# Kernel tuning notes

Hardware: AMD Instinct MI355X
Metric: run time of the kernel (lower is better)

## Reference

```python
import jax, jax.numpy as jnp
import numpy as np

B, DIM, CH = 4, 128, 256      # dim=channels[0], channel=channels[1]
H = W = 256                   # high-res spatial
H0 = W0 = 128                 # low-res spatial (H/2)
NH = 8                        # num_heads
HD = DIM // NH                # head_dim = 16
RD = HD // 2                  # DANE reduction=2 -> 8


def _ln(x, g, b, eps=1e-5):
    m = x.mean(-1, keepdims=True)
    v = ((x - m) ** 2).mean(-1, keepdims=True)
    return (x - m) * jax.lax.rsqrt(v + eps) * g + b


def setup_inputs() -> dict:
    key = jax.random.key(0)
    ks = jax.random.split(key, 14)
    f = lambda k, s: jax.random.normal(k, s, jnp.float32) * 0.02
    return dict(
        x_l=jax.random.normal(ks[0], (B, CH, H0, W0), jnp.float32),
        x_r=jax.random.normal(ks[1], (B, CH, H0, W0), jnp.float32),
        x_l_high=jax.random.normal(ks[2], (B, DIM, H, W), jnp.float32),
        x_r_high=jax.random.normal(ks[3], (B, DIM, H, W), jnp.float32),
        Wq=f(ks[4], (DIM, DIM)), bq=jnp.zeros((DIM,), jnp.float32),
        Wqv=f(ks[5], (DIM, DIM)), bqv=jnp.zeros((DIM,), jnp.float32),
        Wk=f(ks[6], (DIM, CH)), bk=jnp.zeros((DIM,), jnp.float32),
        Wv=f(ks[7], (DIM, CH)), bv=jnp.zeros((DIM,), jnp.float32),
        Wp=f(ks[8], (DIM, DIM)), bp=jnp.zeros((DIM,), jnp.float32),
        ln_g=jnp.ones((DIM,), jnp.float32), ln_b=jnp.zeros((DIM,), jnp.float32),
        d_ln1_g=jnp.ones((HD,), jnp.float32), d_ln1_b=jnp.zeros((HD,), jnp.float32),
        d_ws=f(ks[9], (1, HD)),
        d_w1=f(ks[10], (RD, HD)),
        d_ln2_g=jnp.ones((RD,), jnp.float32), d_ln2_b=jnp.zeros((RD,), jnp.float32),
        d_w2=f(ks[11], (HD, RD)),
    )


def _cross_attn(source, target, Wq, bq, Wqv, bqv, Wk, bk, Wv, bv, Wp, bp,
                ln_g, ln_b, d_ln1_g, d_ln1_b, d_ws, d_w1, d_ln2_g, d_ln2_b, d_w2):
    b_, c, hh, ww = source.shape
    _, c0, h0, w0 = target.shape
    n0 = h0 * w0
    h, d = NH, c // NH
    # 2x2 patchify high-res: (B,C,H0,2,W0,2) -> (B,N0,4,C)
    src = source.reshape(b_, c, h0, 2, w0, 2).transpose(0, 2, 4, 3, 5, 1).reshape(b_, n0, 4, c)
    # low-res target as single token per patch: (B,N0,1,C0)
    tgt = target.reshape(b_, c0, n0).transpose(0, 2, 1)[:, :, None, :]
    q = (src @ Wq.T + bq).reshape(b_, n0, 4, h, d).swapaxes(2, 3)   # (B,N0,h,4,d)
    vq = (src @ Wqv.T + bqv).reshape(b_, n0, 4, h, d).swapaxes(2, 3)
    k = (tgt @ Wk.T + bk).reshape(b_, n0, 1, h, d).swapaxes(2, 3)   # (B,N0,h,1,d)
    v = (tgt @ Wv.T + bv).reshape(b_, n0, 1, h, d).swapaxes(2, 3)
    attn = jnp.einsum('bnhqd,bnhkd->bnhqk', q, k) * (d ** -0.5)     # (B,N0,h,4,1)
    attn = jax.nn.softmax(attn, axis=-2)                            # softmax over the 4-patch axis
    # DANE spatial gate: LN + Linear(d->1) on q, averaged over the 4-patch axis
    sm = (_ln(q, d_ln1_g, d_ln1_b) @ d_ws.T).mean(axis=(3, 4))      # (B,N0,h)
    # DANE channel gate: mean of k over N0, then bottleneck MLP
    km = k.mean(axis=1)                                             # (B,h,1,d)
    cm = jax.nn.silu(km @ d_w1.T)
    cm = _ln(cm, d_ln2_g, d_ln2_b) @ d_w2.T                         # (B,h,1,d)
    w_gate = jax.nn.sigmoid(sm[:, :, :, None, None] + cm[:, None])  # (B,N0,h,1,d)
    x = (1.0 - w_gate) * (attn * v) * 4.0 + w_gate * vq             # (B,N0,h,4,d)
    x = x.swapaxes(2, 3).reshape(b_, n0, 4, c)
    x = _ln(x @ Wp.T + bp, ln_g, ln_b)
    # un-patchify back to (B,C,H,W)
    x = x.reshape(b_, h0, w0, 2, 2, c).transpose(0, 5, 1, 3, 2, 4).reshape(b_, c, hh, ww)
    return x


def reference(x_l, x_r, x_l_high, x_r_high, Wq, bq, Wqv, bqv, Wk, bk, Wv, bv, Wp, bp,
              ln_g, ln_b, d_ln1_g, d_ln1_b, d_ws, d_w1, d_ln2_g, d_ln2_b, d_w2):
    w = (Wq, bq, Wqv, bqv, Wk, bk, Wv, bv, Wp, bp, ln_g, ln_b,
         d_ln1_g, d_ln1_b, d_ws, d_w1, d_ln2_g, d_ln2_b, d_w2)
    # PAFM.fuse (eval mode: DropPath=identity, UsePatch=False => patch=Identity)
    out_l = x_l_high + _cross_attn(x_l_high, x_l, *w)
    out_r = x_r_high + _cross_attn(x_r_high, x_r, *w)
    return (out_l, out_r)
```

## Files before the change

### kernel.cpp

```cpp
#include <hip/hip_runtime.h>
#include <hip/hip_bf16.h>
#include <math.h>


typedef short short8 __attribute__((ext_vector_type(8)));
typedef float f32x4 __attribute__((ext_vector_type(4)));

__device__ __forceinline__ unsigned bf16r(float x) {
    unsigned u = __float_as_uint(x);
    return (u + 0x7FFFu + ((u >> 16) & 1u)) >> 16;
}
__device__ __forceinline__ unsigned pack2(float a, float b) {
    return bf16r(a) | (bf16r(b) << 16);
}
__device__ __forceinline__ float ubf(unsigned short h) {
    return __uint_as_float(((unsigned)h) << 16);
}

__global__ __launch_bounds__(256) void mean_kernel(const float* __restrict__ x_l,
                                                   const float* __restrict__ x_r,
                                                   float* __restrict__ ws_mean) {
    int bid = blockIdx.x;
    const float* src = (bid >= 1024) ? x_r : x_l;
    const float* p = src + (size_t)(bid & 1023) * 16384;
    int t = threadIdx.x;
    float acc = 0.f;
    #pragma unroll 4
    for (int i = t; i < 16384; i += 256) acc += p[i];
    #pragma unroll
    for (int off = 32; off > 0; off >>= 1) acc += __shfl_down(acc, off, 64);
    __shared__ float red[4];
    if ((t & 63) == 0) red[t >> 6] = acc;
    __syncthreads();
    if (t == 0) ws_mean[bid] = (red[0] + red[1] + red[2] + red[3]) * (1.f / 16384.f);
}

__global__ __launch_bounds__(128) void cm_kernel(const float* __restrict__ ws_mean,
                                                 float* __restrict__ ws_cm,
                                                 const float* __restrict__ Wk,
                                                 const float* __restrict__ bk,
                                                 const float* __restrict__ d_w1,
                                                 const float* __restrict__ d_ln2_g,
                                                 const float* __restrict__ d_ln2_b,
                                                 const float* __restrict__ d_w2) {
    int sb = blockIdx.x;
    __shared__ float km[128];
    int o = threadIdx.x;
    const float* mu = ws_mean + sb * 256;
    float acc = bk[o];
    for (int c = 0; c < 256; ++c) acc = fmaf(Wk[o * 256 + c], mu[c], acc);
    km[o] = acc;
    __syncthreads();
    int h = o >> 4, d = o & 15;
    float t1[8];
    #pragma unroll
    for (int r = 0; r < 8; ++r) {
        float a = 0.f;
        #pragma unroll
        for (int dd = 0; dd < 16; ++dd) a = fmaf(d_w1[r * 16 + dd], km[h * 16 + dd], a);
        t1[r] = a / (1.f + expf(-a));
    }
    float m = 0.f;
    #pragma unroll
    for (int r = 0; r < 8; ++r) m += t1[r];
    m *= 0.125f;
    float v = 0.f;
    #pragma unroll
    for (int r = 0; r < 8; ++r) { float df = t1[r] - m; v = fmaf(df, df, v); }
    float rstd = rsqrtf(v * 0.125f + 1e-5f);
    float cmv = 0.f;
    #pragma unroll
    for (int r = 0; r < 8; ++r)
        cmv = fmaf((t1[r] - m) * rstd * d_ln2_g[r] + d_ln2_b[r], d_w2[d * 8 + r], cmv);
    ws_cm[sb * 128 + o] = cmv;
}

__global__ __launch_bounds__(256) void wprep(const float* __restrict__ Wq,
                                             const float* __restrict__ Wqv,
                                             const float* __restrict__ Wk,
                                             const float* __restrict__ Wv,
                                             const float* __restrict__ Wp,
                                             unsigned short* __restrict__ wsp) {
    int bid = blockIdx.x, t = threadIdx.x;
    if (bid < 64) {
        const float* src = (bid < 32) ? Wk : Wv;
        unsigned short* dst = wsp + ((bid < 32) ? 0 : 32768);
        int base = (bid & 31) * 1024;
        #pragma unroll
        for (int i = 0; i < 4; ++i) {
            int el = base + t + 256 * i;
            int q = el >> 13, rem = el & 8191, op = rem >> 8, col = rem & 255;
            dst[q * 8192 + op * 256 + (col ^ ((op & 7) << 3))] =
                (unsigned short)bf16r(src[(q * 32 + op) * 256 + col]);
        }
    } else {
        int g = (bid - 64) >> 4;
        const float* src = (g == 0) ? Wq : (g == 1) ? Wqv : Wp;
        unsigned short* dst = wsp + 65536 + g * 16384;
        int base = ((bid - 64) & 15) * 1024;
        #pragma unroll
        for (int i = 0; i < 4; ++i) {
            int el = base + t + 256 * i;
            int hf = el >> 13, rem = el & 8191, op = rem >> 7, col = rem & 127;
            dst[hf * 8192 + op * 128 + (col ^ ((op & 7) << 3))] =
                (unsigned short)bf16r(src[(hf * 64 + op) * 128 + col]);
        }
    }
}

#define O_XH0 0
#define O_XH1 16384
#define O_XC  32768
#define O_WB  49152
#define O_K   57344
#define O_V   65536
#define O_LG  73728
#define O_SM  75776
#define LDS_U16 76800

__device__ __forceinline__ short8 frag(const unsigned short* lds, int off, int row, int k, int C2) {
    return *(const short8*)&lds[off + row * C2 + (k ^ ((row & 7) << 3))];
}

template<int R, int C2>
__device__ __forceinline__ void stageA(const float* __restrict__ g, size_t cstride,
                                       unsigned short* lds, int off, int t) {
    #pragma unroll
    for (int it = 0; it < (R * (C2 / 2)) / 512; ++it) {
        int idx = t + it * 512;
        int rr = idx & (R - 1);
        int cp = idx / R;
        float a0 = g[(size_t)(2 * cp) * cstride + rr];
        float a1 = g[(size_t)(2 * cp + 1) * cstride + rr];
        int col = (2 * cp) ^ ((rr & 7) << 3);
        *(unsigned*)&lds[off + rr * C2 + col] = pack2(a0, a1);
    }
}

__device__ __forceinline__ void stageW16(const unsigned short* __restrict__ src,
                                         unsigned short* lds, int t) {
    #pragma unroll
    for (int c = 0; c < 2; ++c) {
        int u = (c * 512 + t) * 8;
        *(short8*)&lds[O_WB + u] = *(const short8*)&src[u];
    }
}

#define ZERO4(A) do { _Pragma("unroll") for (int z_ = 0; z_ < 4; ++z_) A[z_] = (f32x4){0.f,0.f,0.f,0.f}; } while (0)

#define KVQ(WOFF, BIAS, OBASE, ODST) do {                                          \
    stageW16(wsp + (WOFF), lds, t);                                                \
    __syncthreads();                                                               \
    f32x4 a_ = (f32x4){0.f,0.f,0.f,0.f};                                           \
    int nt_ = w >> 2, mt_ = w & 3;                                                 \
    _Pragma("unroll")                                                              \
    for (int kc_ = 0; kc_ < 8; ++kc_) {                                            \
      short8 af_ = frag(lds, O_XH0, 16 * mt_ + lm, kc_ * 32 + lg * 8, 256);        \
      short8 bf_ = frag(lds, O_WB, 16 * nt_ + lm, kc_ * 32 + lg * 8, 256);         \
      a_ = __builtin_amdgcn_mfma_f32_16x16x32_bf16(af_, bf_, a_, 0, 0, 0);         \
    }                                                                              \
    { int o_ = (OBASE) + 16 * nt_ + lm; float bb_ = (BIAS)[o_];                    \
      _Pragma("unroll")                                                            \
      for (int r_ = 0; r_ < 4; ++r_) {                                             \
        int tok_ = 16 * mt_ + 4 * lg + r_;                                         \
        lds[(ODST) + tok_ * 128 + (o_ ^ ((tok_ & 7) << 3))] = (unsigned short)bf16r(a_[r_] + bb_); \
      } }                                                                          \
    __syncthreads();                                                               \
  } while (0)

#define GEMM128(ACC, XOFF) do {                                                    \
    _Pragma("unroll")                                                              \
    for (int kc_ = 0; kc_ < 4; ++kc_) {                                            \
      short8 af_ = frag(lds, (XOFF), 16 * w + lm, kc_ * 32 + lg * 8, 128);         \
      _Pragma("unroll")                                                            \
      for (int n_ = 0; n_ < 4; ++n_) {                                             \
        short8 bf_ = frag(lds, O_WB, 16 * n_ + lm, kc_ * 32 + lg * 8, 128);        \
        ACC[n_] = __builtin_amdgcn_mfma_f32_16x16x32_bf16(af_, bf_, ACC[n_], 0, 0, 0); \
      } }                                                                          \
  } while (0)

#define CONSUME(ACC, DY, NH) do {                                                  \
    _Pragma("unroll")                                                              \
    for (int n_ = 0; n_ < 4; ++n_) {                                               \
      int nt_ = 4 * (NH) + n_;                                                     \
      int o_ = 16 * nt_ + lm;                                                      \
      float bias_ = bq[o_];                                                        \
      float sd01_ = 0.f, sd23_ = 0.f;                                              \
      _Pragma("unroll")                                                            \
      for (int r_ = 0; r_ < 4; ++r_) {                                             \
        int row_ = 16 * w + 4 * lg + r_;                                           \
        int tok_ = row_ >> 1;                                                      \
        float q_ = ACC[n_][r_] + bias_;                                            \
        float kv_ = ubf(lds[O_K + tok_ * 128 + (o_ ^ ((tok_ & 7) << 3))]);         \
        float t0_ = q_, t1_ = q_ * q_, t2_ = q_ * gw, t3_ = q_ * kv_;              \
        _Pragma("unroll")                                                          \
        for (int d_ = 1; d_ < 16; d_ <<= 1) {                                      \
          t0_ += __shfl_xor(t0_, d_, 64); t1_ += __shfl_xor(t1_, d_, 64);          \
          t2_ += __shfl_xor(t2_, d_, 64); t3_ += __shfl_xor(t3_, d_, 64);          \
        }                                                                          \
        float mn_ = t0_ * 0.0625f;                                                 \
        float rs_ = rsqrtf(t1_ * 0.0625f - mn_ * mn_ + 1e-5f);                     \
        float sdt_ = rs_ * (t2_ - mn_ * S1) + S2;                                  \
        if (r_ < 2) sd01_ += sdt_; else sd23_ += sdt_;                             \
        if (lm == r_) lds[O_LG + ((DY) * 128 + row_) * 8 + nt_] = (unsigned short)bf16r(t3_ * 0.25f); \
      }                                                                            \
      if (lm == 0) smf[(8 * w + 2 * lg) * 8 + nt_]     += sd01_;                   \
      if (lm == 1) smf[(8 * w + 2 * lg + 1) * 8 + nt_] += sd23_;                   \
    } } while (0)

#define COMBINE(ACC, DY, NH) do {                                                  \
    _Pragma("unroll")                                                              \
    for (int n_ = 0; n_ < 4; ++n_) {                                               \
      int nt_ = 4 * (NH) + n_;                                                     \
      int o_ = 16 * nt_ + lm;                                                      \
      float bias_ = bqv[o_];                                                       \
      float cmv_ = cmp[o_];                                                        \
      _Pragma("unroll")                                                            \
      for (int r_ = 0; r_ < 4; ++r_) {                                             \
        int row_ = 16 * w + 4 * lg + r_;                                           \
        int jj_ = row_ >> 1;                                                       \
        float vq_ = ACC[n_][r_] + bias_;                                           \
        float aw_ = ubf(lds[O_LG + ((DY) * 128 + row_) * 8 + nt_]);                \
        float vv_ = ubf(lds[O_V + jj_ * 128 + (o_ ^ ((jj_ & 7) << 3))]);           \
        float wg_ = 1.f / (1.f + __expf(-(smf[jj_ * 8 + nt_] + cmv_)));            \
        float xc_ = (1.f - wg_) * aw_ * vv_ * 4.f + wg_ * vq_;                     \
        lds[O_XC + row_ * 128 + (o_ ^ ((row_ & 7) << 3))] = (unsigned short)bf16r(xc_); \
      } } } while (0)

__global__ __launch_bounds__(512, 2) void pafm_v5(
    const float* __restrict__ x_l,  const float* __restrict__ x_r,
    const float* __restrict__ x_lh, const float* __restrict__ x_rh,
    const float* __restrict__ bq,   const float* __restrict__ bqv,
    const float* __restrict__ bk,   const float* __restrict__ bv,
    const float* __restrict__ bp,
    const float* __restrict__ ln_g, const float* __restrict__ ln_b,
    const float* __restrict__ d_ln1_g, const float* __restrict__ d_ln1_b,
    const float* __restrict__ d_wsv,
    const float* __restrict__ ws_cm,
    const unsigned short* __restrict__ wsp,
    float* __restrict__ out) {

    __shared__ unsigned short lds[LDS_U16];
    float* smf = (float*)&lds[O_SM];

    int bid = blockIdx.x;
    int s  = bid >> 10;
    int b  = (bid >> 8) & 3;
    int i0 = (bid >> 1) & 127;
    int j0 = (bid & 1) * 64;

    int t = threadIdx.x, w = t >> 6, l = t & 63, lm = l & 15, lg = l >> 4;

    const float* xlow  = s ? x_r  : x_l;
    const float* xhigh = s ? x_rh : x_lh;
    const float* cmp   = ws_cm + (s * 4 + b) * 128;

    float gw = d_ln1_g[lm] * d_wsv[lm];
    float S1 = gw, S2 = d_ln1_b[lm] * d_wsv[lm];
    #pragma unroll
    for (int d = 1; d < 16; d <<= 1) { S1 += __shfl_xor(S1, d, 64); S2 += __shfl_xor(S2, d, 64); }

    const float* lowb = xlow + ((size_t)(b * 256) * 128 + i0) * 128 + j0;

    smf[t & 511] = 0.f;

    stageA<64, 256>(lowb, 16384, lds, O_XH0, t);
    __syncthreads();
    KVQ(0,     bk, 0,  O_K); KVQ(8192,  bk, 32, O_K);
    KVQ(16384, bk, 64, O_K); KVQ(24576, bk, 96, O_K);
    KVQ(32768, bv, 0,  O_V); KVQ(40960, bv, 32, O_V);
    KVQ(49152, bv, 64, O_V); KVQ(57344, bv, 96, O_V);

    {
        const float* hb0 = xhigh + ((size_t)(b * 128) * 256 + (2 * i0)) * 256 + 2 * j0;
        const float* hb1 = hb0 + 256;
        stageA<128, 128>(hb0, 65536, lds, O_XH0, t);
        stageA<128, 128>(hb1, 65536, lds, O_XH1, t);
    }
    __syncthreads();

    {
        stageW16(wsp + 65536, lds, t);
        __syncthreads();
        { f32x4 q4[4]; ZERO4(q4); GEMM128(q4, O_XH0); CONSUME(q4, 0, 0); }
        { f32x4 q4[4]; ZERO4(q4); GEMM128(q4, O_XH1); CONSUME(q4, 1, 0); }
        __syncthreads();
        stageW16(wsp + 65536 + 8192, lds, t);
        __syncthreads();
        { f32x4 q4[4]; ZERO4(q4); GEMM128(q4, O_XH0); CONSUME(q4, 0, 1); }
        { f32x4 q4[4]; ZERO4(q4); GEMM128(q4, O_XH1); CONSUME(q4, 1, 1); }
        __syncthreads();
    }

    {
        int jj = t >> 3, h = t & 7;
        int r00 = (2 * jj) * 8 + h,       r01 = (2 * jj + 1) * 8 + h;
        int r10 = (128 + 2 * jj) * 8 + h, r11 = (128 + 2 * jj + 1) * 8 + h;
        float l00 = ubf(lds[O_LG + r00]), l01 = ubf(lds[O_LG + r01]);
        float l10 = ubf(lds[O_LG + r10]), l11 = ubf(lds[O_LG + r11]);
        float mx = fmaxf(fmaxf(l00, l01), fmaxf(l10, l11));
        float e00 = __expf(l00 - mx), e01 = __expf(l01 - mx);
        float e10 = __expf(l10 - mx), e11 = __expf(l11 - mx);
        float inv = 1.f / (e00 + e01 + e10 + e11);
        lds[O_LG + r00] = (unsigned short)bf16r(e00 * inv);
        lds[O_LG + r01] = (unsigned short)bf16r(e01 * inv);
        lds[O_LG + r10] = (unsigned short)bf16r(e10 * inv);
        lds[O_LG + r11] = (unsigned short)bf16r(e11 * inv);
        smf[jj * 8 + h] *= 0.25f;
    }
    __syncthreads();

    for (int dy = 0; dy < 2; ++dy) {
        int xoff = dy ? O_XH1 : O_XH0;
        stageW16(wsp + 81920, lds, t);
        __syncthreads();
        { f32x4 v4_[4]; ZERO4(v4_); GEMM128(v4_, xoff); COMBINE(v4_, dy, 0); }
        __syncthreads();
        stageW16(wsp + 81920 + 8192, lds, t);
        __syncthreads();
        { f32x4 v4_[4]; ZERO4(v4_); GEMM128(v4_, xoff); COMBINE(v4_, dy, 1); }
        __syncthreads();

        f32x4 pA[4], pB[4];
        stageW16(wsp + 98304, lds, t);
        __syncthreads();
        ZERO4(pA); GEMM128(pA, O_XC);
        __syncthreads();
        stageW16(wsp + 98304 + 8192, lds, t);
        __syncthreads();
        ZERO4(pB); GEMM128(pB, O_XC);
        __syncthreads();

        float mean_[4], rstd_[4];
        #pragma unroll
        for (int r = 0; r < 4; ++r) {
            float ps = 0.f, pq = 0.f;
            #pragma unroll
            for (int n = 0; n < 4; ++n) {
                float y0 = pA[n][r] + bp[16 * n + lm];
                float y1 = pB[n][r] + bp[64 + 16 * n + lm];
                ps += y0 + y1;
                pq = fmaf(y0, y0, pq); pq = fmaf(y1, y1, pq);
            }
            #pragma unroll
            for (int d = 1; d < 16; d <<= 1) { ps += __shfl_xor(ps, d, 64); pq += __shfl_xor(pq, d, 64); }
            float mn = ps * (1.f / 128.f);
            mean_[r] = mn;
            rstd_[r] = rsqrtf(pq * (1.f / 128.f) - mn * mn + 1e-5f);
        }
        #pragma unroll
        for (int n = 0; n < 4; ++n) {
            int oA = 16 * n + lm, oB = 64 + 16 * n + lm;
            float gA = ln_g[oA], bA = ln_b[oA], biA = bp[oA];
            float gB = ln_g[oB], bB = ln_b[oB], biB = bp[oB];
            #pragma unroll
            for (int r = 0; r < 4; ++r) {
                int row = 16 * w + 4 * lg + r;
                float ynA = (pA[n][r] + biA - mean_[r]) * rstd_[r] * gA + bA;
                float ynB = (pB[n][r] + biB - mean_[r]) * rstd_[r] * gB + bB;
                lds[O_XC + row * 128 + (oA ^ ((row & 31) << 2))] = (unsigned short)bf16r(ynA);
                lds[O_XC + row * 128 + (oB ^ ((row & 31) << 2))] = (unsigned short)bf16r(ynB);
            }
        }
        __syncthreads();
        {
            float* ob = out + (size_t)s * 33554432
                      + ((size_t)(b * 128)) * 65536 + (size_t)(2 * i0 + dy) * 256 + 2 * j0;
            int ph = t & 127, oq = t >> 7;
            #pragma unroll 8
            for (int it = 0; it < 32; ++it) {
                int oo = 4 * it + oq;
                float yn = ubf(lds[O_XC + ph * 128 + (oo ^ ((ph & 31) << 2))]);
                float xh = ubf(lds[xoff + ph * 128 + (oo ^ ((ph & 7) << 3))]);
                ob[(size_t)oo * 65536 + ph] = xh + yn;
            }
        }
        __syncthreads();
    }
}

extern "C" void kernel_launch(void* const* d_in, const int* in_sizes, int n_in,
                              void* d_out, int out_size, void* d_ws, size_t ws_size,
                              hipStream_t stream) {
    const float* x_l   = (const float*)d_in[0];
    const float* x_r   = (const float*)d_in[1];
    const float* x_lh  = (const float*)d_in[2];
    const float* x_rh  = (const float*)d_in[3];
    const float* Wq    = (const float*)d_in[4];
    const float* bq    = (const float*)d_in[5];
    const float* Wqv   = (const float*)d_in[6];
    const float* bqv   = (const float*)d_in[7];
    const float* Wk    = (const float*)d_in[8];
    const float* bk    = (const float*)d_in[9];
    const float* Wv    = (const float*)d_in[10];
    const float* bv    = (const float*)d_in[11];
    const float* Wp    = (const float*)d_in[12];
    const float* bp    = (const float*)d_in[13];
    const float* ln_g  = (const float*)d_in[14];
    const float* ln_b  = (const float*)d_in[15];
    const float* dln1g = (const float*)d_in[16];
    const float* dln1b = (const float*)d_in[17];
    const float* d_wsv = (const float*)d_in[18];
    const float* d_w1  = (const float*)d_in[19];
    const float* dln2g = (const float*)d_in[20];
    const float* dln2b = (const float*)d_in[21];
    const float* d_w2  = (const float*)d_in[22];

    float* out = (float*)d_out;
    float* ws_mean = (float*)d_ws;
    float* ws_cm   = ws_mean + 2048;
    unsigned short* wsp = (unsigned short*)((char*)d_ws + 16384);

    mean_kernel<<<2048, 256, 0, stream>>>(x_l, x_r, ws_mean);
    wprep<<<112, 256, 0, stream>>>(Wq, Wqv, Wk, Wv, Wp, wsp);
    cm_kernel<<<8, 128, 0, stream>>>(ws_mean, ws_cm, Wk, bk, d_w1, dln2g, dln2b, d_w2);
    pafm_v5<<<2048, 512, 0, stream>>>(x_l, x_r, x_lh, x_rh,
                                      bq, bqv, bk, bv, bp, ln_g, ln_b,
                                      dln1g, dln1b, d_wsv, ws_cm, wsp, out);
}
```

Measured before the change: 610.7 us.

## Read weights from global memory and shrink LDS to raise occupancy

```diff
diff --git a/kernel.cpp b/kernel.cpp
--- a/kernel.cpp
+++ b/kernel.cpp
@@ -5,6 +5,7 @@
 
 typedef short short8 __attribute__((ext_vector_type(8)));
 typedef float f32x4 __attribute__((ext_vector_type(4)));
+typedef unsigned uint4v __attribute__((ext_vector_type(4)));
 
 __device__ __forceinline__ unsigned bf16r(float x) {
     unsigned u = __float_as_uint(x);
@@ -108,76 +109,42 @@
     }
 }
 
-#define O_XH0 0
-#define O_XH1 16384
-#define O_XC  32768
-#define O_WB  49152
-#define O_K   57344
-#define O_V   65536
-#define O_LG  73728
-#define O_SM  75776
-#define LDS_U16 76800
+#define O_XA 0
+#define O_K  16384
+#define O_V  24576
+#define O_LG 32768
+#define O_SM 34816
+#define LDS_U16 35840
 
 __device__ __forceinline__ short8 frag(const unsigned short* lds, int off, int row, int k, int C2) {
     return *(const short8*)&lds[off + row * C2 + (k ^ ((row & 7) << 3))];
 }
+__device__ __forceinline__ short8 wfrag(const unsigned short* __restrict__ p, int row, int k, int C2) {
+    return *(const short8*)&p[row * C2 + (k ^ ((row & 7) << 3))];
+}
 
 template<int R, int C2>
-__device__ __forceinline__ void stageA(const float* __restrict__ g, size_t cstride,
-                                       unsigned short* lds, int off, int t) {
-    #pragma unroll
-    for (int it = 0; it < (R * (C2 / 2)) / 512; ++it) {
+__device__ __forceinline__ void stageA16(const float* __restrict__ g, size_t cstride,
+                                         unsigned short* lds, int off, int t) {
+    #pragma unroll
+    for (int it = 0; it < (R * (C2 / 8)) / 512; ++it) {
         int idx = t + it * 512;
         int rr = idx & (R - 1);
-        int cp = idx / R;
-        float a0 = g[(size_t)(2 * cp) * cstride + rr];
-        float a1 = g[(size_t)(2 * cp + 1) * cstride + rr];
-        int col = (2 * cp) ^ ((rr & 7) << 3);
-        *(unsigned*)&lds[off + rr * C2 + col] = pack2(a0, a1);
-    }
-}
-
-__device__ __forceinline__ void stageW16(const unsigned short* __restrict__ src,
-                                         unsigned short* lds, int t) {
-    #pragma unroll
-    for (int c = 0; c < 2; ++c) {
-        int u = (c * 512 + t) * 8;
-        *(short8*)&lds[O_WB + u] = *(const short8*)&src[u];
+        int bc = idx / R;
+        float v0 = g[(size_t)(8 * bc + 0) * cstride + rr];
+        float v1 = g[(size_t)(8 * bc + 1) * cstride + rr];
+        float v2 = g[(size_t)(8 * bc + 2) * cstride + rr];
+        float v3 = g[(size_t)(8 * bc + 3) * cstride + rr];
+        float v4 = g[(size_t)(8 * bc + 4) * cstride + rr];
+        float v5 = g[(size_t)(8 * bc + 5) * cstride + rr];
+        float v6 = g[(size_t)(8 * bc + 6) * cstride + rr];
+        float v7 = g[(size_t)(8 * bc + 7) * cstride + rr];
+        uint4v u = {pack2(v0, v1), pack2(v2, v3), pack2(v4, v5), pack2(v6, v7)};
+        *(uint4v*)&lds[off + rr * C2 + ((bc ^ (rr & 7)) << 3)] = u;
     }
 }
 
 #define ZERO4(A) do { _Pragma("unroll") for (int z_ = 0; z_ < 4; ++z_) A[z_] = (f32x4){0.f,0.f,0.f,0.f}; } while (0)
-
-#define KVQ(WOFF, BIAS, OBASE, ODST) do {                                          \
-    stageW16(wsp + (WOFF), lds, t);                                                \
-    __syncthreads();                                                               \
-    f32x4 a_ = (f32x4){0.f,0.f,0.f,0.f};                                           \
-    int nt_ = w >> 2, mt_ = w & 3;                                                 \
-    _Pragma("unroll")                                                              \
-    for (int kc_ = 0; kc_ < 8; ++kc_) {                                            \
-      short8 af_ = frag(lds, O_XH0, 16 * mt_ + lm, kc_ * 32 + lg * 8, 256);        \
-      short8 bf_ = frag(lds, O_WB, 16 * nt_ + lm, kc_ * 32 + lg * 8, 256);         \
-      a_ = __builtin_amdgcn_mfma_f32_16x16x32_bf16(af_, bf_, a_, 0, 0, 0);         \
-    }                                                                              \
-    { int o_ = (OBASE) + 16 * nt_ + lm; float bb_ = (BIAS)[o_];                    \
-      _Pragma("unroll")                                                            \
-      for (int r_ = 0; r_ < 4; ++r_) {                                             \
-        int tok_ = 16 * mt_ + 4 * lg + r_;                                         \
-        lds[(ODST) + tok_ * 128 + (o_ ^ ((tok_ & 7) << 3))] = (unsigned short)bf16r(a_[r_] + bb_); \
-      } }                                                                          \
-    __syncthreads();                                                               \
-  } while (0)
-
-#define GEMM128(ACC, XOFF) do {                                                    \
-    _Pragma("unroll")                                                              \
-    for (int kc_ = 0; kc_ < 4; ++kc_) {                                            \
-      short8 af_ = frag(lds, (XOFF), 16 * w + lm, kc_ * 32 + lg * 8, 128);         \
-      _Pragma("unroll")                                                            \
-      for (int n_ = 0; n_ < 4; ++n_) {                                             \
-        short8 bf_ = frag(lds, O_WB, 16 * n_ + lm, kc_ * 32 + lg * 8, 128);        \
-        ACC[n_] = __builtin_amdgcn_mfma_f32_16x16x32_bf16(af_, bf_, ACC[n_], 0, 0, 0); \
-      } }                                                                          \
-  } while (0)
 
 #define CONSUME(ACC, DY, NH) do {                                                  \
     _Pragma("unroll")                                                              \
@@ -224,10 +191,10 @@
         float vv_ = ubf(lds[O_V + jj_ * 128 + (o_ ^ ((jj_ & 7) << 3))]);           \
         float wg_ = 1.f / (1.f + __expf(-(smf[jj_ * 8 + nt_] + cmv_)));            \
         float xc_ = (1.f - wg_) * aw_ * vv_ * 4.f + wg_ * vq_;                     \
-        lds[O_XC + row_ * 128 + (o_ ^ ((row_ & 7) << 3))] = (unsigned short)bf16r(xc_); \
+        lds[O_XA + row_ * 128 + (o_ ^ ((row_ & 7) << 3))] = (unsigned short)bf16r(xc_); \
       } } } while (0)
 
-__global__ __launch_bounds__(512, 2) void pafm_v5(
+__global__ __launch_bounds__(512, 4) void pafm_v6(
     const float* __restrict__ x_l,  const float* __restrict__ x_r,
     const float* __restrict__ x_lh, const float* __restrict__ x_rh,
     const float* __restrict__ bq,   const float* __restrict__ bqv,
@@ -261,36 +228,59 @@
     for (int d = 1; d < 16; d <<= 1) { S1 += __shfl_xor(S1, d, 64); S2 += __shfl_xor(S2, d, 64); }
 
     const float* lowb = xlow + ((size_t)(b * 256) * 128 + i0) * 128 + j0;
+    const float* hbase = xhigh + ((size_t)(b * 128) * 256 + 2 * i0) * 256 + 2 * j0;
 
     smf[t & 511] = 0.f;
 
-    stageA<64, 256>(lowb, 16384, lds, O_XH0, t);
+    stageA16<64, 256>(lowb, 16384, lds, O_XA, t);
     __syncthreads();
-    KVQ(0,     bk, 0,  O_K); KVQ(8192,  bk, 32, O_K);
-    KVQ(16384, bk, 64, O_K); KVQ(24576, bk, 96, O_K);
-    KVQ(32768, bv, 0,  O_V); KVQ(40960, bv, 32, O_V);
-    KVQ(49152, bv, 64, O_V); KVQ(57344, bv, 96, O_V);
-
     {
-        const float* hb0 = xhigh + ((size_t)(b * 128) * 256 + (2 * i0)) * 256 + 2 * j0;
-        const float* hb1 = hb0 + 256;
-        stageA<128, 128>(hb0, 65536, lds, O_XH0, t);
-        stageA<128, 128>(hb1, 65536, lds, O_XH1, t);
+        int nt = w >> 2, mt = w & 3;
+        #pragma unroll
+        for (int q = 0; q < 4; ++q) {
+            f32x4 aK = (f32x4){0.f,0.f,0.f,0.f}, aV = (f32x4){0.f,0.f,0.f,0.f};
+            #pragma unroll
+            for (int kc = 0; kc < 8; ++kc) {
+                short8 af = frag(lds, O_XA, 16 * mt + lm, kc * 32 + lg * 8, 256);
+                aK = __builtin_amdgcn_mfma_f32_16x16x32_bf16(
+                        af, wfrag(wsp + q * 8192, 16 * nt + lm, kc * 32 + lg * 8, 256), aK, 0, 0, 0);
+                aV = __builtin_amdgcn_mfma_f32_16x16x32_bf16(
+                        af, wfrag(wsp + 32768 + q * 8192, 16 * nt + lm, kc * 32 + lg * 8, 256), aV, 0, 0, 0);
+            }
+            int o = q * 32 + 16 * nt + lm;
+            float bbk = bk[o], bbv = bv[o];
+            #pragma unroll
+            for (int r = 0; r < 4; ++r) {
+                int tok = 16 * mt + 4 * lg + r;
+                lds[O_K + tok * 128 + (o ^ ((tok & 7) << 3))] = (unsigned short)bf16r(aK[r] + bbk);
+                lds[O_V + tok * 128 + (o ^ ((tok & 7) << 3))] = (unsigned short)bf16r(aV[r] + bbv);
+            }
+        }
+    }
+
+    #pragma unroll 1
+    for (int dy = 0; dy < 2; ++dy) {
+        __syncthreads();
+        stageA16<128, 128>(hbase + dy * 256, 65536, lds, O_XA, t);
+        __syncthreads();
+        f32x4 qA[4], qB[4];
+        ZERO4(qA); ZERO4(qB);
+        #pragma unroll
+        for (int kc = 0; kc < 4; ++kc) {
+            short8 af = frag(lds, O_XA, 16 * w + lm, kc * 32 + lg * 8, 128);
+            #pragma unroll
+            for (int n = 0; n < 4; ++n)
+                qA[n] = __builtin_amdgcn_mfma_f32_16x16x32_bf16(
+                          af, wfrag(wsp + 65536, 16 * n + lm, kc * 32 + lg * 8, 128), qA[n], 0, 0, 0);
+            #pragma unroll
+            for (int n = 0; n < 4; ++n)
+                qB[n] = __builtin_amdgcn_mfma_f32_16x16x32_bf16(
+                          af, wfrag(wsp + 65536 + 8192, 16 * n + lm, kc * 32 + lg * 8, 128), qB[n], 0, 0, 0);
+        }
+        CONSUME(qA, dy, 0);
+        CONSUME(qB, dy, 1);
     }
     __syncthreads();
-
-    {
-        stageW16(wsp + 65536, lds, t);
-        __syncthreads();
-        { f32x4 q4[4]; ZERO4(q4); GEMM128(q4, O_XH0); CONSUME(q4, 0, 0); }
-        { f32x4 q4[4]; ZERO4(q4); GEMM128(q4, O_XH1); CONSUME(q4, 1, 0); }
-        __syncthreads();
-        stageW16(wsp + 65536 + 8192, lds, t);
-        __syncthreads();
-        { f32x4 q4[4]; ZERO4(q4); GEMM128(q4, O_XH0); CONSUME(q4, 0, 1); }
-        { f32x4 q4[4]; ZERO4(q4); GEMM128(q4, O_XH1); CONSUME(q4, 1, 1); }
-        __syncthreads();
-    }
 
     {
         int jj = t >> 3, h = t & 7;
@@ -310,25 +300,43 @@
     }
     __syncthreads();
 
+    #pragma unroll 1
     for (int dy = 0; dy < 2; ++dy) {
-        int xoff = dy ? O_XH1 : O_XH0;
-        stageW16(wsp + 81920, lds, t);
-        __syncthreads();
-        { f32x4 v4_[4]; ZERO4(v4_); GEMM128(v4_, xoff); COMBINE(v4_, dy, 0); }
-        __syncthreads();
-        stageW16(wsp + 81920 + 8192, lds, t);
-        __syncthreads();
-        { f32x4 v4_[4]; ZERO4(v4_); GEMM128(v4_, xoff); COMBINE(v4_, dy, 1); }
+        stageA16<128, 128>(hbase + dy * 256, 65536, lds, O_XA, t);
+        __syncthreads();
+        f32x4 vqA[4], vqB[4];
+        ZERO4(vqA); ZERO4(vqB);
+        #pragma unroll
+        for (int kc = 0; kc < 4; ++kc) {
+            short8 af = frag(lds, O_XA, 16 * w + lm, kc * 32 + lg * 8, 128);
+            #pragma unroll
+            for (int n = 0; n < 4; ++n)
+                vqA[n] = __builtin_amdgcn_mfma_f32_16x16x32_bf16(
+                           af, wfrag(wsp + 81920, 16 * n + lm, kc * 32 + lg * 8, 128), vqA[n], 0, 0, 0);
+            #pragma unroll
+            for (int n = 0; n < 4; ++n)
+                vqB[n] = __builtin_amdgcn_mfma_f32_16x16x32_bf16(
+                           af, wfrag(wsp + 81920 + 8192, 16 * n + lm, kc * 32 + lg * 8, 128), vqB[n], 0, 0, 0);
+        }
+        __syncthreads();
+        COMBINE(vqA, dy, 0);
+        COMBINE(vqB, dy, 1);
         __syncthreads();
 
         f32x4 pA[4], pB[4];
-        stageW16(wsp + 98304, lds, t);
-        __syncthreads();
-        ZERO4(pA); GEMM128(pA, O_XC);
-        __syncthreads();
-        stageW16(wsp + 98304 + 8192, lds, t);
-        __syncthreads();
-        ZERO4(pB); GEMM128(pB, O_XC);
+        ZERO4(pA); ZERO4(pB);
+        #pragma unroll
+        for (int kc = 0; kc < 4; ++kc) {
+            short8 af = frag(lds, O_XA, 16 * w + lm, kc * 32 + lg * 8, 128);
+            #pragma unroll
+            for (int n = 0; n < 4; ++n)
+                pA[n] = __builtin_amdgcn_mfma_f32_16x16x32_bf16(
+                          af, wfrag(wsp + 98304, 16 * n + lm, kc * 32 + lg * 8, 128), pA[n], 0, 0, 0);
+            #pragma unroll
+            for (int n = 0; n < 4; ++n)
+                pB[n] = __builtin_amdgcn_mfma_f32_16x16x32_bf16(
+                          af, wfrag(wsp + 98304 + 8192, 16 * n + lm, kc * 32 + lg * 8, 128), pB[n], 0, 0, 0);
+        }
         __syncthreads();
 
         float mean_[4], rstd_[4];
@@ -358,24 +366,27 @@
                 int row = 16 * w + 4 * lg + r;
                 float ynA = (pA[n][r] + biA - mean_[r]) * rstd_[r] * gA + bA;
                 float ynB = (pB[n][r] + biB - mean_[r]) * rstd_[r] * gB + bB;
-                lds[O_XC + row * 128 + (oA ^ ((row & 31) << 2))] = (unsigned short)bf16r(ynA);
-                lds[O_XC + row * 128 + (oB ^ ((row & 31) << 2))] = (unsigned short)bf16r(ynB);
+                lds[O_XA + row * 128 + ((((oA >> 1) ^ (row & 31)) << 1) | (oA & 1))] = (unsigned short)bf16r(ynA);
+                lds[O_XA + row * 128 + ((((oB >> 1) ^ (row & 31)) << 1) | (oB & 1))] = (unsigned short)bf16r(ynB);
             }
         }
         __syncthreads();
         {
+            const float* rb = hbase + dy * 256;
             float* ob = out + (size_t)s * 33554432
                       + ((size_t)(b * 128)) * 65536 + (size_t)(2 * i0 + dy) * 256 + 2 * j0;
-            int ph = t & 127, oq = t >> 7;
-            #pragma unroll 8
-            for (int it = 0; it < 32; ++it) {
-                int oo = 4 * it + oq;
-                float yn = ubf(lds[O_XC + ph * 128 + (oo ^ ((ph & 31) << 2))]);
-                float xh = ubf(lds[xoff + ph * 128 + (oo ^ ((ph & 7) << 3))]);
-                ob[(size_t)oo * 65536 + ph] = xh + yn;
+            int ph = t & 127, cq = t >> 7;
+            #pragma unroll
+            for (int it = 0; it < 16; ++it) {
+                int c4 = it * 4 + cq;
+                unsigned uv = *(const unsigned*)&lds[O_XA + ph * 128 + ((c4 ^ (ph & 31)) << 1)];
+                size_t off0 = (size_t)(2 * c4) * 65536 + ph;
+                size_t off1 = off0 + 65536;
+                ob[off0] = rb[off0] + ubf((unsigned short)(uv & 0xFFFF));
+                ob[off1] = rb[off1] + ubf((unsigned short)(uv >> 16));
             }
         }
-        __syncthreads();
+        if (dy == 0) __syncthreads();
     }
 }
 
@@ -414,7 +425,7 @@
     mean_kernel<<<2048, 256, 0, stream>>>(x_l, x_r, ws_mean);
     wprep<<<112, 256, 0, stream>>>(Wq, Wqv, Wk, Wv, Wp, wsp);
     cm_kernel<<<8, 128, 0, stream>>>(ws_mean, ws_cm, Wk, bk, d_w1, dln2g, dln2b, d_w2);
-    pafm_v5<<<2048, 512, 0, stream>>>(x_l, x_r, x_lh, x_rh,
+    pafm_v6<<<2048, 512, 0, stream>>>(x_l, x_r, x_lh, x_rh,
                                       bq, bqv, bk, bv, bp, ln_g, ln_b,
                                       dln1g, dln1b, d_wsv, ws_cm, wsp, out);
 }
```

Measured after the change: 2.050 ms. +235.6%, slower.
